# Kernel optimization log

Measured on AMD Instinct MI355X. Metric: run time of the kernel, lower is better.

## Reference

```python
import jax, jax.numpy as jnp
import numpy as np

DIM = 256
WH, WW = 7, 7
N = WH * WW
HEADS = 8
HEAD_DIM = DIM // HEADS
SCALE = HEAD_DIM ** -0.5
B_ = 4096
NW = 64  # windows per image; B_ % NW == 0


def _relative_position_index():
    coords = np.stack(np.meshgrid(np.arange(WH), np.arange(WW), indexing='ij'))  # (2,Wh,Ww)
    flat = coords.reshape(2, -1)  # (2,N)
    rel = flat[:, :, None] - flat[:, None, :]  # (2,N,N)
    rel = rel.transpose(1, 2, 0)  # (N,N,2)
    rel = rel + np.array([WH - 1, WW - 1])
    rel = rel * np.array([2 * WW - 1, 1])
    return rel.sum(-1).astype(np.int32)  # (N,N)


def setup_inputs() -> dict:
    key = jax.random.key(0)
    ks = jax.random.split(key, 7)
    num_rel = (2 * WH - 1) * (2 * WW - 1)
    return {
        'x': jax.random.normal(ks[0], (B_, N, DIM), jnp.float32),
        'mask': jax.random.normal(ks[1], (NW, N, N), jnp.float32),
        'qkv_w': jax.random.normal(ks[2], (DIM, 3 * DIM), jnp.float32) * 0.02,
        'qkv_b': jnp.zeros((3 * DIM,), jnp.float32),
        'proj_w': jax.random.normal(ks[3], (DIM, DIM), jnp.float32) * 0.02,
        'proj_b': jnp.zeros((DIM,), jnp.float32),
        'bias_table': jax.random.normal(ks[4], (num_rel, HEADS), jnp.float32) * 0.02,
        'rel_index': jnp.asarray(_relative_position_index()),
    }


def reference(x, mask, qkv_w, qkv_b, proj_w, proj_b, bias_table, rel_index):
    B, n, C = x.shape
    qkv = x @ qkv_w + qkv_b  # (B,N,3C)
    qkv = qkv.reshape(B, n, 3, HEADS, HEAD_DIM).transpose(2, 0, 3, 1, 4)
    q, k, v = qkv[0], qkv[1], qkv[2]  # (B,H,N,hd)
    attn = jnp.einsum('bhnd,bhmd->bhnm', q * SCALE, k)  # (B,H,N,N)
    rel_bias = bias_table[rel_index.reshape(-1)].reshape(n, n, HEADS)
    attn = attn + rel_bias.transpose(2, 0, 1)[None]  # (B,H,N,N)
    nW = mask.shape[0]
    attn = attn.reshape(-1, nW, HEADS, n, n) + mask[None, :, None]
    attn = attn.reshape(-1, HEADS, n, n)
    attn = jax.nn.softmax(attn, axis=-1)
    out = jnp.einsum('bhnm,bhmd->bhnd', attn, v)  # (B,H,N,hd)
    out = out.transpose(0, 2, 1, 3).reshape(B, n, C)
    return out @ proj_w + proj_b
```

## Files before the change

### kernel.cpp

```cpp
#include <hip/hip_runtime.h>
#include <hip/hip_bf16.h>


#define NTOK 49
static constexpr float SCALE_Q = 0.17677669529663687f;

using bf16   = __bf16;
using bf16x4 = __attribute__((ext_vector_type(4))) __bf16;
using bf16x8 = __attribute__((ext_vector_type(8))) __bf16;
using short4v = __attribute__((ext_vector_type(4))) short;
using f32x4  = __attribute__((ext_vector_type(4))) float;

#define WT_QKV_OFF 0
#define WT_PROJ_OFF (768 * 256 * 2)
#define SB_OFF (WT_PROJ_OFF + 256 * 256 * 2)
#define SM_OFF (SB_OFF + 8 * 4096 * 4)
#define WS_NEEDED (SM_OFF + (size_t)64 * 4096 * 4)

static __device__ __forceinline__ f32x4 mfma16(bf16x4 a, bf16x4 b, f32x4 c) {
#if __has_builtin(__builtin_amdgcn_mfma_f32_16x16x16_bf16)
    return __builtin_amdgcn_mfma_f32_16x16x16_bf16(a, b, c, 0, 0, 0);
#elif __has_builtin(__builtin_amdgcn_mfma_f32_16x16x16bf16_1k)
    return __builtin_amdgcn_mfma_f32_16x16x16bf16_1k(
        __builtin_bit_cast(short4v, a), __builtin_bit_cast(short4v, b), c, 0, 0, 0);
#elif __has_builtin(__builtin_amdgcn_mfma_f32_16x16x16_bf16_1k)
    return __builtin_amdgcn_mfma_f32_16x16x16_bf16_1k(
        __builtin_bit_cast(short4v, a), __builtin_bit_cast(short4v, b), c, 0, 0, 0);
#else
    asm volatile("v_mfma_f32_16x16x16_bf16 %0, %1, %2, %0\n\t"
                 "s_nop 7\n\ts_nop 7\n\ts_nop 1"
                 : "+v"(c) : "v"(a), "v"(b));
    return c;
#endif
}

__global__ void prep_wqkv(const float* __restrict__ qkv_w, bf16* __restrict__ wt) {
    int idx = blockIdx.x * 256 + threadIdx.x;
    if (idx >= 768 * 256) return;
    int n = idx >> 8, k = idx & 255;
    float v = qkv_w[k * 768 + n];
    if (n < 256) v *= SCALE_Q;
    wt[idx] = (bf16)v;
}
__global__ void prep_wproj(const float* __restrict__ proj_w, bf16* __restrict__ wt) {
    int idx = blockIdx.x * 256 + threadIdx.x;
    if (idx >= 256 * 256) return;
    int n = idx >> 8, k = idx & 255;
    wt[idx] = (bf16)proj_w[k * 256 + n];
}
__global__ void prep_sb(const float* __restrict__ bias_table, const int* __restrict__ rel_index,
                        float* __restrict__ sb) {
    int idx = blockIdx.x * 256 + threadIdx.x;
    if (idx >= 8 * 4096) return;
    int r    = idx & 3;
    int lane = (idx >> 2) & 63;
    int qp   = (idx >> 8) & 15;
    int h    = idx >> 12;
    int kt = qp >> 2, qt = qp & 3;
    int i = qt * 16 + (lane & 15);
    int j = kt * 16 + (lane >> 4) * 4 + r;
    float v;
    if (j >= NTOK)      v = -1e30f;
    else if (i >= NTOK) v = 0.0f;
    else v = bias_table[rel_index[i * 49 + j] * 8 + h];
    sb[idx] = v;
}
__global__ void prep_sm(const float* __restrict__ mask, float* __restrict__ sm) {
    int idx = blockIdx.x * 256 + threadIdx.x;
    if (idx >= 64 * 4096) return;
    int r    = idx & 3;
    int lane = (idx >> 2) & 63;
    int qp   = (idx >> 8) & 15;
    int w    = idx >> 12;
    int kt = qp >> 2, qt = qp & 3;
    int i = qt * 16 + (lane & 15);
    int j = kt * 16 + (lane >> 4) * 4 + r;
    sm[idx] = (i < NTOK && j < NTOK) ? mask[(w * 49 + i) * 49 + j] : 0.0f;
}

__global__ __launch_bounds__(512, 2) void fused_attn(
    const float* __restrict__ x,
    const float* __restrict__ qkv_b,
    const float* __restrict__ proj_b,
    const bf16* __restrict__ wt_qkv,
    const bf16* __restrict__ wt_proj,
    const float* __restrict__ sb,
    const float* __restrict__ sm,
    float* __restrict__ out)
{
    __shared__ char xs[32768];
    const int b    = blockIdx.x;
    const int tid  = threadIdx.x;
    const int lane = tid & 63;
    const int h    = tid >> 6;
    const int c    = lane & 15;
    const int g    = lane >> 4;

    {
        const float* xb = x + (size_t)b * (NTOK * 256);
        float4 xr[8];
        #pragma unroll
        for (int it = 0; it < 8; ++it) {
            int idx = it * 512 + tid;
            int row = idx >> 6, c4 = idx & 63;
            xr[it] = make_float4(0.f, 0.f, 0.f, 0.f);
            if (row < NTOK) xr[it] = ((const float4*)xb)[row * 64 + c4];
        }
        #pragma unroll
        for (int it = 0; it < 8; ++it) {
            int idx = it * 512 + tid;
            int row = idx >> 6, c4 = idx & 63;
            bf16x4 o;
            o[0] = (bf16)xr[it].x; o[1] = (bf16)xr[it].y;
            o[2] = (bf16)xr[it].z; o[3] = (bf16)xr[it].w;
            *(bf16x4*)(xs + row * 512 + ((c4 * 8) ^ ((row & 7) << 4))) = o;
        }
    }
    __syncthreads();

    bf16x4 iden;
    #pragma unroll
    for (int j = 0; j < 4; ++j) iden[j] = (bf16)((4 * g + j == c) ? 1.0f : 0.0f);

    bf16x4 qf[4][2];
    bf16x4 kf[4][2];
    bf16x4 vf[2][4];

    {
        f32x4 acc[4][4];
        #pragma unroll
        for (int ni = 0; ni < 4; ++ni)
            #pragma unroll
            for (int mi = 0; mi < 4; ++mi)
                acc[ni][mi] = (f32x4){0.f, 0.f, 0.f, 0.f};

        #pragma unroll
        for (int kk = 0; kk < 8; ++kk) {
            bf16x8 bb[4];
            #pragma unroll
            for (int ni = 0; ni < 4; ++ni) {
                int ncol = (ni >> 1) * 256 + h * 32 + (ni & 1) * 16 + c;
                bb[ni] = *(const bf16x8*)(wt_qkv + ncol * 256 + kk * 32 + g * 8);
            }
            bf16x8 a[4];
            #pragma unroll
            for (int mi = 0; mi < 4; ++mi) {
                int row = mi * 16 + c;
                a[mi] = *(const bf16x8*)(xs + row * 512 + ((kk * 64 + g * 16) ^ ((row & 7) << 4)));
            }
            #pragma unroll
            for (int ni = 0; ni < 4; ++ni)
                #pragma unroll
                for (int mi = 0; mi < 4; ++mi)
                    acc[ni][mi] = __builtin_amdgcn_mfma_f32_16x16x32_bf16(a[mi], bb[ni], acc[ni][mi], 0, 0, 0);
        }
        #pragma unroll
        for (int ni = 0; ni < 4; ++ni) {
            int col = (ni >> 1) * 256 + h * 32 + (ni & 1) * 16 + c;
            float bias = qkv_b[col];
            if (ni < 2) bias *= SCALE_Q;
            #pragma unroll
            for (int mi = 0; mi < 4; ++mi) {
                bf16x4 in;
                #pragma unroll
                for (int r = 0; r < 4; ++r) in[r] = (bf16)(acc[ni][mi][r] + bias);
                f32x4 t = mfma16(in, iden, (f32x4){0.f, 0.f, 0.f, 0.f});
                bf16x4 o;
                #pragma unroll
                for (int r = 0; r < 4; ++r) o[r] = (bf16)t[r];
                if (ni < 2) qf[mi][ni] = o;
                else        kf[mi][ni - 2] = o;
            }
        }
    }

    {
        f32x4 acc[2][4];
        #pragma unroll
        for (int dt = 0; dt < 2; ++dt)
            #pragma unroll
            for (int mi = 0; mi < 4; ++mi)
                acc[dt][mi] = (f32x4){0.f, 0.f, 0.f, 0.f};

        #pragma unroll
        for (int kk = 0; kk < 8; ++kk) {
            bf16x8 bv[2];
            #pragma unroll
            for (int dt = 0; dt < 2; ++dt) {
                int ncol = 512 + h * 32 + dt * 16 + c;
                bv[dt] = *(const bf16x8*)(wt_qkv + ncol * 256 + kk * 32 + g * 8);
            }
            bf16x8 a[4];
            #pragma unroll
            for (int mi = 0; mi < 4; ++mi) {
                int row = mi * 16 + c;
                a[mi] = *(const bf16x8*)(xs + row * 512 + ((kk * 64 + g * 16) ^ ((row & 7) << 4)));
            }
            #pragma unroll
            for (int dt = 0; dt < 2; ++dt)
                #pragma unroll
                for (int mi = 0; mi < 4; ++mi)
                    acc[dt][mi] = __builtin_amdgcn_mfma_f32_16x16x32_bf16(a[mi], bv[dt], acc[dt][mi], 0, 0, 0);
        }
        #pragma unroll
        for (int dt = 0; dt < 2; ++dt) {
            float vb = qkv_b[512 + h * 32 + dt * 16 + c];
            #pragma unroll
            for (int kt = 0; kt < 4; ++kt)
                #pragma unroll
                for (int r = 0; r < 4; ++r) vf[dt][kt][r] = (bf16)(acc[dt][kt][r] + vb);
        }
    }
    __syncthreads();

    const float* sbh = sb + (size_t)h * 4096;
    const float* smw = sm + (size_t)(b & 63) * 4096;
    #pragma unroll
    for (int qt = 0; qt < 4; ++qt) {
        f32x4 sbv[4], smv[4];
        #pragma unroll
        for (int kt = 0; kt < 4; ++kt)
            sbv[kt] = *(const f32x4*)(sbh + (kt * 4 + qt) * 256 + lane * 4);
        #pragma unroll
        for (int kt = 0; kt < 4; ++kt)
            smv[kt] = *(const f32x4*)(smw + (kt * 4 + qt) * 256 + lane * 4);

        f32x4 sT[4];
        __builtin_amdgcn_s_setprio(1);
        #pragma unroll
        for (int kt = 0; kt < 4; ++kt) {
            sT[kt] = (f32x4){0.f, 0.f, 0.f, 0.f};
            sT[kt] = mfma16(kf[kt][0], qf[qt][0], sT[kt]);
            sT[kt] = mfma16(kf[kt][1], qf[qt][1], sT[kt]);
        }
        __builtin_amdgcn_s_setprio(0);
        #pragma unroll
        for (int kt = 0; kt < 4; ++kt)
            #pragma unroll
            for (int r = 0; r < 4; ++r)
                sT[kt][r] += sbv[kt][r] + smv[kt][r];
        float m = sT[0][0];
        #pragma unroll
        for (int kt = 0; kt < 4; ++kt)
            #pragma unroll
            for (int r = 0; r < 4; ++r) m = fmaxf(m, sT[kt][r]);
        m = fmaxf(m, __shfl_xor(m, 16));
        m = fmaxf(m, __shfl_xor(m, 32));
        float sum = 0.f;
        #pragma unroll
        for (int kt = 0; kt < 4; ++kt)
            #pragma unroll
            for (int r = 0; r < 4; ++r) {
                float e = __expf(sT[kt][r] - m);
                sT[kt][r] = e;
                sum += e;
            }
        sum += __shfl_xor(sum, 16);
        sum += __shfl_xor(sum, 32);
        float rs = 1.f / sum;
        bf16x4 pB[4];
        #pragma unroll
        for (int kt = 0; kt < 4; ++kt)
            #pragma unroll
            for (int r = 0; r < 4; ++r) pB[kt][r] = (bf16)(sT[kt][r] * rs);
        __builtin_amdgcn_s_setprio(1);
        #pragma unroll
        for (int dt = 0; dt < 2; ++dt) {
            f32x4 oT = (f32x4){0.f, 0.f, 0.f, 0.f};
            #pragma unroll
            for (int kt = 0; kt < 4; ++kt)
                oT = mfma16(vf[dt][kt], pB[kt], oT);
            int row = qt * 16 + c;
            int cbyte = h * 64 + dt * 32 + g * 8;
            bf16x4 o;
            #pragma unroll
            for (int r = 0; r < 4; ++r) o[r] = (bf16)oT[r];
            *(bf16x4*)(xs + row * 512 + (cbyte ^ ((row & 7) << 4))) = o;
        }
        __builtin_amdgcn_s_setprio(0);
    }
    __syncthreads();

    {
        f32x4 po[2][4];
        #pragma unroll
        for (int ni = 0; ni < 2; ++ni)
            #pragma unroll
            for (int mi = 0; mi < 4; ++mi)
                po[ni][mi] = (f32x4){0.f, 0.f, 0.f, 0.f};

        #pragma unroll
        for (int kk = 0; kk < 8; ++kk) {
            bf16x8 bw[2];
            #pragma unroll
            for (int ni = 0; ni < 2; ++ni) {
                int col = h * 32 + ni * 16 + c;
                bw[ni] = *(const bf16x8*)(wt_proj + col * 256 + kk * 32 + g * 8);
            }
            bf16x8 a[4];
            #pragma unroll
            for (int mi = 0; mi < 4; ++mi) {
                int row = mi * 16 + c;
                a[mi] = *(const bf16x8*)(xs + row * 512 + ((kk * 64 + g * 16) ^ ((row & 7) << 4)));
            }
            #pragma unroll
            for (int ni = 0; ni < 2; ++ni)
                #pragma unroll
                for (int mi = 0; mi < 4; ++mi)
                    po[ni][mi] = __builtin_amdgcn_mfma_f32_16x16x32_bf16(a[mi], bw[ni], po[ni][mi], 0, 0, 0);
        }
        float* outb = out + (size_t)b * (NTOK * 256);
        #pragma unroll
        for (int ni = 0; ni < 2; ++ni) {
            int col = h * 32 + ni * 16 + c;
            float pb = proj_b[col];
            #pragma unroll
            for (int mi = 0; mi < 4; ++mi) {
                #pragma unroll
                for (int r = 0; r < 4; ++r) {
                    int row = mi * 16 + g * 4 + r;
                    if (row < NTOK) outb[row * 256 + col] = po[ni][mi][r] + pb;
                }
            }
        }
    }
}

extern "C" void kernel_launch(void* const* d_in, const int* in_sizes, int n_in,
                              void* d_out, int out_size, void* d_ws, size_t ws_size,
                              hipStream_t stream) {
    const float* x          = (const float*)d_in[0];
    const float* mask       = (const float*)d_in[1];
    const float* qkv_w      = (const float*)d_in[2];
    const float* qkv_b      = (const float*)d_in[3];
    const float* proj_w     = (const float*)d_in[4];
    const float* proj_b     = (const float*)d_in[5];
    const float* bias_table = (const float*)d_in[6];
    const int*   rel_index  = (const int*)d_in[7];
    float* out = (float*)d_out;

    if (ws_size < WS_NEEDED) return;

    char* ws = (char*)d_ws;
    bf16*  wt_qkv  = (bf16*)(ws + WT_QKV_OFF);
    bf16*  wt_proj = (bf16*)(ws + WT_PROJ_OFF);
    float* sbp     = (float*)(ws + SB_OFF);
    float* smp     = (float*)(ws + SM_OFF);

    prep_wqkv <<<768, 256, 0, stream>>>(qkv_w, wt_qkv);
    prep_wproj<<<256, 256, 0, stream>>>(proj_w, wt_proj);
    prep_sb   <<<128, 256, 0, stream>>>(bias_table, rel_index, sbp);
    prep_sm   <<<1024, 256, 0, stream>>>(mask, smp);

    fused_attn<<<4096, 512, 0, stream>>>(x, qkv_b, proj_b, wt_qkv, wt_proj, sbp, smp, out);
}
```

Measured before the change: 394.3 us.

## Use 256-thread blocks with each wave processing two heads

Halves the block to 4 waves, and each wave now loops over two attention heads, keeping their outputs in registers until a single LDS write-back before the projection GEMM. The projection GEMM gives each wave 64 output columns instead of 32. Launch bounds change to (256,4), so more blocks can be resident per CU for the same 32KB LDS each. The cost is more register pressure from holding two heads' outputs and per-wave serial work, which may cause spills.

```diff
diff --git a/kernel.cpp b/kernel.cpp
--- a/kernel.cpp
+++ b/kernel.cpp
@@ -78,7 +78,7 @@
     sm[idx] = (i < NTOK && j < NTOK) ? mask[(w * 49 + i) * 49 + j] : 0.0f;
 }
 
-__global__ __launch_bounds__(512, 2) void fused_attn(
+__global__ __launch_bounds__(256, 4) void fused_attn(
     const float* __restrict__ x,
     const float* __restrict__ qkv_b,
     const float* __restrict__ proj_b,
@@ -92,28 +92,31 @@
     const int b    = blockIdx.x;
     const int tid  = threadIdx.x;
     const int lane = tid & 63;
-    const int h    = tid >> 6;
+    const int wv   = tid >> 6;
     const int c    = lane & 15;
     const int g    = lane >> 4;
 
     {
         const float* xb = x + (size_t)b * (NTOK * 256);
-        float4 xr[8];
-        #pragma unroll
-        for (int it = 0; it < 8; ++it) {
-            int idx = it * 512 + tid;
-            int row = idx >> 6, c4 = idx & 63;
-            xr[it] = make_float4(0.f, 0.f, 0.f, 0.f);
-            if (row < NTOK) xr[it] = ((const float4*)xb)[row * 64 + c4];
-        }
-        #pragma unroll
-        for (int it = 0; it < 8; ++it) {
-            int idx = it * 512 + tid;
-            int row = idx >> 6, c4 = idx & 63;
-            bf16x4 o;
-            o[0] = (bf16)xr[it].x; o[1] = (bf16)xr[it].y;
-            o[2] = (bf16)xr[it].z; o[3] = (bf16)xr[it].w;
-            *(bf16x4*)(xs + row * 512 + ((c4 * 8) ^ ((row & 7) << 4))) = o;
+        #pragma unroll
+        for (int bt = 0; bt < 2; ++bt) {
+            float4 xr[8];
+            #pragma unroll
+            for (int it = 0; it < 8; ++it) {
+                int idx = bt * 2048 + it * 256 + tid;
+                int row = idx >> 6, c4 = idx & 63;
+                xr[it] = make_float4(0.f, 0.f, 0.f, 0.f);
+                if (row < NTOK) xr[it] = ((const float4*)xb)[row * 64 + c4];
+            }
+            #pragma unroll
+            for (int it = 0; it < 8; ++it) {
+                int idx = bt * 2048 + it * 256 + tid;
+                int row = idx >> 6, c4 = idx & 63;
+                bf16x4 o;
+                o[0] = (bf16)xr[it].x; o[1] = (bf16)xr[it].y;
+                o[2] = (bf16)xr[it].z; o[3] = (bf16)xr[it].w;
+                *(bf16x4*)(xs + row * 512 + ((c4 * 8) ^ ((row & 7) << 4))) = o;
+            }
         }
     }
     __syncthreads();
@@ -122,25 +125,197 @@
     #pragma unroll
     for (int j = 0; j < 4; ++j) iden[j] = (bf16)((4 * g + j == c) ? 1.0f : 0.0f);
 
-    bf16x4 qf[4][2];
-    bf16x4 kf[4][2];
-    bf16x4 vf[2][4];
+    bf16x4 ob[2][2][4];
+
+    #pragma unroll
+    for (int hh = 0; hh < 2; ++hh) {
+        const int h = wv + hh * 4;
+
+        bf16x4 qf[4][2];
+        bf16x4 kf[4][2];
+        bf16x4 vf[2][4];
+
+        {
+            f32x4 acc[4][4];
+            #pragma unroll
+            for (int ni = 0; ni < 4; ++ni)
+                #pragma unroll
+                for (int mi = 0; mi < 4; ++mi)
+                    acc[ni][mi] = (f32x4){0.f, 0.f, 0.f, 0.f};
+
+            #pragma unroll
+            for (int kk = 0; kk < 8; ++kk) {
+                bf16x8 bb[4];
+                #pragma unroll
+                for (int ni = 0; ni < 4; ++ni) {
+                    int ncol = (ni >> 1) * 256 + h * 32 + (ni & 1) * 16 + c;
+                    bb[ni] = *(const bf16x8*)(wt_qkv + ncol * 256 + kk * 32 + g * 8);
+                }
+                bf16x8 a[4];
+                #pragma unroll
+                for (int mi = 0; mi < 4; ++mi) {
+                    int row = mi * 16 + c;
+                    a[mi] = *(const bf16x8*)(xs + row * 512 + ((kk * 64 + g * 16) ^ ((row & 7) << 4)));
+                }
+                #pragma unroll
+                for (int ni = 0; ni < 4; ++ni)
+                    #pragma unroll
+                    for (int mi = 0; mi < 4; ++mi)
+                        acc[ni][mi] = __builtin_amdgcn_mfma_f32_16x16x32_bf16(a[mi], bb[ni], acc[ni][mi], 0, 0, 0);
+            }
+            #pragma unroll
+            for (int ni = 0; ni < 4; ++ni) {
+                int col = (ni >> 1) * 256 + h * 32 + (ni & 1) * 16 + c;
+                float bias = qkv_b[col];
+                if (ni < 2) bias *= SCALE_Q;
+                #pragma unroll
+                for (int mi = 0; mi < 4; ++mi) {
+                    bf16x4 in;
+                    #pragma unroll
+                    for (int r = 0; r < 4; ++r) in[r] = (bf16)(acc[ni][mi][r] + bias);
+                    f32x4 t = mfma16(in, iden, (f32x4){0.f, 0.f, 0.f, 0.f});
+                    bf16x4 o;
+                    #pragma unroll
+                    for (int r = 0; r < 4; ++r) o[r] = (bf16)t[r];
+                    if (ni < 2) qf[mi][ni] = o;
+                    else        kf[mi][ni - 2] = o;
+                }
+            }
+        }
+
+        {
+            f32x4 acc[2][4];
+            #pragma unroll
+            for (int dt = 0; dt < 2; ++dt)
+                #pragma unroll
+                for (int mi = 0; mi < 4; ++mi)
+                    acc[dt][mi] = (f32x4){0.f, 0.f, 0.f, 0.f};
+
+            #pragma unroll
+            for (int kk = 0; kk < 8; ++kk) {
+                bf16x8 bv[2];
+                #pragma unroll
+                for (int dt = 0; dt < 2; ++dt) {
+                    int ncol = 512 + h * 32 + dt * 16 + c;
+                    bv[dt] = *(const bf16x8*)(wt_qkv + ncol * 256 + kk * 32 + g * 8);
+                }
+                bf16x8 a[4];
+                #pragma unroll
+                for (int mi = 0; mi < 4; ++mi) {
+                    int row = mi * 16 + c;
+                    a[mi] = *(const bf16x8*)(xs + row * 512 + ((kk * 64 + g * 16) ^ ((row & 7) << 4)));
+                }
+                #pragma unroll
+                for (int dt = 0; dt < 2; ++dt)
+                    #pragma unroll
+                    for (int mi = 0; mi < 4; ++mi)
+                        acc[dt][mi] = __builtin_amdgcn_mfma_f32_16x16x32_bf16(a[mi], bv[dt], acc[dt][mi], 0, 0, 0);
+            }
+            #pragma unroll
+            for (int dt = 0; dt < 2; ++dt) {
+                float vb = qkv_b[512 + h * 32 + dt * 16 + c];
+                #pragma unroll
+                for (int kt = 0; kt < 4; ++kt)
+                    #pragma unroll
+                    for (int r = 0; r < 4; ++r) vf[dt][kt][r] = (bf16)(acc[dt][kt][r] + vb);
+            }
+        }
+
+        const float* sbh = sb + (size_t)h * 4096;
+        const float* smw = sm + (size_t)(b & 63) * 4096;
+        #pragma unroll
+        for (int qt = 0; qt < 4; ++qt) {
+            f32x4 sbv[4], smv[4];
+            #pragma unroll
+            for (int kt = 0; kt < 4; ++kt)
+                sbv[kt] = *(const f32x4*)(sbh + (kt * 4 + qt) * 256 + lane * 4);
+            #pragma unroll
+            for (int kt = 0; kt < 4; ++kt)
+                smv[kt] = *(const f32x4*)(smw + (kt * 4 + qt) * 256 + lane * 4);
+
+            f32x4 sT[4];
+            __builtin_amdgcn_s_setprio(1);
+            #pragma unroll
+            for (int kt = 0; kt < 4; ++kt) {
+                sT[kt] = (f32x4){0.f, 0.f, 0.f, 0.f};
+                sT[kt] = mfma16(kf[kt][0], qf[qt][0], sT[kt]);
+                sT[kt] = mfma16(kf[kt][1], qf[qt][1], sT[kt]);
+            }
+            __builtin_amdgcn_s_setprio(0);
+            #pragma unroll
+            for (int kt = 0; kt < 4; ++kt)
+                #pragma unroll
+                for (int r = 0; r < 4; ++r)
+                    sT[kt][r] += sbv[kt][r] + smv[kt][r];
+            float m = sT[0][0];
+            #pragma unroll
+            for (int kt = 0; kt < 4; ++kt)
+                #pragma unroll
+                for (int r = 0; r < 4; ++r) m = fmaxf(m, sT[kt][r]);
+            m = fmaxf(m, __shfl_xor(m, 16));
+            m = fmaxf(m, __shfl_xor(m, 32));
+            float sum = 0.f;
+            #pragma unroll
+            for (int kt = 0; kt < 4; ++kt)
+                #pragma unroll
+                for (int r = 0; r < 4; ++r) {
+                    float e = __expf(sT[kt][r] - m);
+                    sT[kt][r] = e;
+                    sum += e;
+                }
+            sum += __shfl_xor(sum, 16);
+            sum += __shfl_xor(sum, 32);
+            float rs = 1.f / sum;
+            bf16x4 pB[4];
+            #pragma unroll
+            for (int kt = 0; kt < 4; ++kt)
+                #pragma unroll
+                for (int r = 0; r < 4; ++r) pB[kt][r] = (bf16)(sT[kt][r] * rs);
+            __builtin_amdgcn_s_setprio(1);
+            #pragma unroll
+            for (int dt = 0; dt < 2; ++dt) {
+                f32x4 oT = (f32x4){0.f, 0.f, 0.f, 0.f};
+                #pragma unroll
+                for (int kt = 0; kt < 4; ++kt)
+                    oT = mfma16(vf[dt][kt], pB[kt], oT);
+                #pragma unroll
+                for (int r = 0; r < 4; ++r) ob[hh][dt][qt][r] = (bf16)oT[r];
+            }
+            __builtin_amdgcn_s_setprio(0);
+        }
+    }
+    __syncthreads();
+
+    #pragma unroll
+    for (int hh = 0; hh < 2; ++hh) {
+        int h = wv + hh * 4;
+        #pragma unroll
+        for (int qt = 0; qt < 4; ++qt) {
+            int row = qt * 16 + c;
+            #pragma unroll
+            for (int dt = 0; dt < 2; ++dt) {
+                int cbyte = h * 64 + dt * 32 + g * 8;
+                *(bf16x4*)(xs + row * 512 + (cbyte ^ ((row & 7) << 4))) = ob[hh][dt][qt];
+            }
+        }
+    }
+    __syncthreads();
 
     {
-        f32x4 acc[4][4];
+        f32x4 po[4][4];
         #pragma unroll
         for (int ni = 0; ni < 4; ++ni)
             #pragma unroll
             for (int mi = 0; mi < 4; ++mi)
-                acc[ni][mi] = (f32x4){0.f, 0.f, 0.f, 0.f};
+                po[ni][mi] = (f32x4){0.f, 0.f, 0.f, 0.f};
 
         #pragma unroll
         for (int kk = 0; kk < 8; ++kk) {
-            bf16x8 bb[4];
+            bf16x8 bw[4];
             #pragma unroll
             for (int ni = 0; ni < 4; ++ni) {
-                int ncol = (ni >> 1) * 256 + h * 32 + (ni & 1) * 16 + c;
-                bb[ni] = *(const bf16x8*)(wt_qkv + ncol * 256 + kk * 32 + g * 8);
+                int col = wv * 64 + ni * 16 + c;
+                bw[ni] = *(const bf16x8*)(wt_proj + col * 256 + kk * 32 + g * 8);
             }
             bf16x8 a[4];
             #pragma unroll
@@ -152,167 +327,12 @@
             for (int ni = 0; ni < 4; ++ni)
                 #pragma unroll
                 for (int mi = 0; mi < 4; ++mi)
-                    acc[ni][mi] = __builtin_amdgcn_mfma_f32_16x16x32_bf16(a[mi], bb[ni], acc[ni][mi], 0, 0, 0);
-        }
+                    po[ni][mi] = __builtin_amdgcn_mfma_f32_16x16x32_bf16(a[mi], bw[ni], po[ni][mi], 0, 0, 0);
+        }
+        float* outb = out + (size_t)b * (NTOK * 256);
         #pragma unroll
         for (int ni = 0; ni < 4; ++ni) {
-            int col = (ni >> 1) * 256 + h * 32 + (ni & 1) * 16 + c;
-            float bias = qkv_b[col];
-            if (ni < 2) bias *= SCALE_Q;
-            #pragma unroll
-            for (int mi = 0; mi < 4; ++mi) {
-                bf16x4 in;
-                #pragma unroll
-                for (int r = 0; r < 4; ++r) in[r] = (bf16)(acc[ni][mi][r] + bias);
-                f32x4 t = mfma16(in, iden, (f32x4){0.f, 0.f, 0.f, 0.f});
-                bf16x4 o;
-                #pragma unroll
-                for (int r = 0; r < 4; ++r) o[r] = (bf16)t[r];
-                if (ni < 2) qf[mi][ni] = o;
-                else        kf[mi][ni - 2] = o;
-            }
-        }
-    }
-
-    {
-        f32x4 acc[2][4];
-        #pragma unroll
-        for (int dt = 0; dt < 2; ++dt)
-            #pragma unroll
-            for (int mi = 0; mi < 4; ++mi)
-                acc[dt][mi] = (f32x4){0.f, 0.f, 0.f, 0.f};
-
-        #pragma unroll
-        for (int kk = 0; kk < 8; ++kk) {
-            bf16x8 bv[2];
-            #pragma unroll
-            for (int dt = 0; dt < 2; ++dt) {
-                int ncol = 512 + h * 32 + dt * 16 + c;
-                bv[dt] = *(const bf16x8*)(wt_qkv + ncol * 256 + kk * 32 + g * 8);
-            }
-            bf16x8 a[4];
-            #pragma unroll
-            for (int mi = 0; mi < 4; ++mi) {
-                int row = mi * 16 + c;
-                a[mi] = *(const bf16x8*)(xs + row * 512 + ((kk * 64 + g * 16) ^ ((row & 7) << 4)));
-            }
-            #pragma unroll
-            for (int dt = 0; dt < 2; ++dt)
-                #pragma unroll
-                for (int mi = 0; mi < 4; ++mi)
-                    acc[dt][mi] = __builtin_amdgcn_mfma_f32_16x16x32_bf16(a[mi], bv[dt], acc[dt][mi], 0, 0, 0);
-        }
-        #pragma unroll
-        for (int dt = 0; dt < 2; ++dt) {
-            float vb = qkv_b[512 + h * 32 + dt * 16 + c];
-            #pragma unroll
-            for (int kt = 0; kt < 4; ++kt)
-                #pragma unroll
-                for (int r = 0; r < 4; ++r) vf[dt][kt][r] = (bf16)(acc[dt][kt][r] + vb);
-        }
-    }
-    __syncthreads();
-
-    const float* sbh = sb + (size_t)h * 4096;
-    const float* smw = sm + (size_t)(b & 63) * 4096;
-    #pragma unroll
-    for (int qt = 0; qt < 4; ++qt) {
-        f32x4 sbv[4], smv[4];
-        #pragma unroll
-        for (int kt = 0; kt < 4; ++kt)
-            sbv[kt] = *(const f32x4*)(sbh + (kt * 4 + qt) * 256 + lane * 4);
-        #pragma unroll
-        for (int kt = 0; kt < 4; ++kt)
-            smv[kt] = *(const f32x4*)(smw + (kt * 4 + qt) * 256 + lane * 4);
-
-        f32x4 sT[4];
-        __builtin_amdgcn_s_setprio(1);
-        #pragma unroll
-        for (int kt = 0; kt < 4; ++kt) {
-            sT[kt] = (f32x4){0.f, 0.f, 0.f, 0.f};
-            sT[kt] = mfma16(kf[kt][0], qf[qt][0], sT[kt]);
-            sT[kt] = mfma16(kf[kt][1], qf[qt][1], sT[kt]);
-        }
-        __builtin_amdgcn_s_setprio(0);
-        #pragma unroll
-        for (int kt = 0; kt < 4; ++kt)
-            #pragma unroll
-            for (int r = 0; r < 4; ++r)
-                sT[kt][r] += sbv[kt][r] + smv[kt][r];
-        float m = sT[0][0];
-        #pragma unroll
-        for (int kt = 0; kt < 4; ++kt)
-            #pragma unroll
-            for (int r = 0; r < 4; ++r) m = fmaxf(m, sT[kt][r]);
-        m = fmaxf(m, __shfl_xor(m, 16));
-        m = fmaxf(m, __shfl_xor(m, 32));
-        float sum = 0.f;
-        #pragma unroll
-        for (int kt = 0; kt < 4; ++kt)
-            #pragma unroll
-            for (int r = 0; r < 4; ++r) {
-                float e = __expf(sT[kt][r] - m);
-                sT[kt][r] = e;
-                sum += e;
-            }
-        sum += __shfl_xor(sum, 16);
-        sum += __shfl_xor(sum, 32);
-        float rs = 1.f / sum;
-        bf16x4 pB[4];
-        #pragma unroll
-        for (int kt = 0; kt < 4; ++kt)
-            #pragma unroll
-            for (int r = 0; r < 4; ++r) pB[kt][r] = (bf16)(sT[kt][r] * rs);
-        __builtin_amdgcn_s_setprio(1);
-        #pragma unroll
-        for (int dt = 0; dt < 2; ++dt) {
-            f32x4 oT = (f32x4){0.f, 0.f, 0.f, 0.f};
-            #pragma unroll
-            for (int kt = 0; kt < 4; ++kt)
-                oT = mfma16(vf[dt][kt], pB[kt], oT);
-            int row = qt * 16 + c;
-            int cbyte = h * 64 + dt * 32 + g * 8;
-            bf16x4 o;
-            #pragma unroll
-            for (int r = 0; r < 4; ++r) o[r] = (bf16)oT[r];
-            *(bf16x4*)(xs + row * 512 + (cbyte ^ ((row & 7) << 4))) = o;
-        }
-        __builtin_amdgcn_s_setprio(0);
-    }
-    __syncthreads();
-
-    {
-        f32x4 po[2][4];
-        #pragma unroll
-        for (int ni = 0; ni < 2; ++ni)
-            #pragma unroll
-            for (int mi = 0; mi < 4; ++mi)
-                po[ni][mi] = (f32x4){0.f, 0.f, 0.f, 0.f};
-
-        #pragma unroll
-        for (int kk = 0; kk < 8; ++kk) {
-            bf16x8 bw[2];
-            #pragma unroll
-            for (int ni = 0; ni < 2; ++ni) {
-                int col = h * 32 + ni * 16 + c;
-                bw[ni] = *(const bf16x8*)(wt_proj + col * 256 + kk * 32 + g * 8);
-            }
-            bf16x8 a[4];
-            #pragma unroll
-            for (int mi = 0; mi < 4; ++mi) {
-                int row = mi * 16 + c;
-                a[mi] = *(const bf16x8*)(xs + row * 512 + ((kk * 64 + g * 16) ^ ((row & 7) << 4)));
-            }
-            #pragma unroll
-            for (int ni = 0; ni < 2; ++ni)
-                #pragma unroll
-                for (int mi = 0; mi < 4; ++mi)
-                    po[ni][mi] = __builtin_amdgcn_mfma_f32_16x16x32_bf16(a[mi], bw[ni], po[ni][mi], 0, 0, 0);
-        }
-        float* outb = out + (size_t)b * (NTOK * 256);
-        #pragma unroll
-        for (int ni = 0; ni < 2; ++ni) {
-            int col = h * 32 + ni * 16 + c;
+            int col = wv * 64 + ni * 16 + c;
             float pb = proj_b[col];
             #pragma unroll
             for (int mi = 0; mi < 4; ++mi) {
@@ -352,5 +372,5 @@
     prep_sb   <<<128, 256, 0, stream>>>(bias_table, rel_index, sbp);
     prep_sm   <<<1024, 256, 0, stream>>>(mask, smp);
 
-    fused_attn<<<4096, 512, 0, stream>>>(x, qkv_b, proj_b, wt_qkv, wt_proj, sbp, smp, out);
-}
+    fused_attn<<<4096, 256, 0, stream>>>(x, qkv_b, proj_b, wt_qkv, wt_proj, sbp, smp, out);
+}
```

Measured after the change: 915.7 us. +132.2%, slower.
